# Optimization experiments

Hardware: AMD Instinct MI355X
Metric: run time of the kernel (lower is better)

The kernel has to match this reference:

```python
import jax, jax.numpy as jnp
import numpy as np

B, N, T, D, H = 32, 64, 16, 256, 256  # batch, actors, frames, feat dim, hidden_dim


def setup_inputs() -> dict:
    key = jax.random.key(0)
    ks = jax.random.split(key, 6)
    s = lambda fan: 1.0 / np.sqrt(fan)
    return {
        "x": jax.random.normal(ks[0], (B, N, T, D), jnp.float32),
        "W1_t": jax.random.normal(ks[1], (T * D, H), jnp.float32) * s(T * D),
        "b1_t": jnp.zeros((H,), jnp.float32),
        "W2_t": jax.random.normal(ks[2], (H, H), jnp.float32) * s(H),
        "b2_t": jnp.zeros((H,), jnp.float32),
        "W1_i": jax.random.normal(ks[3], (2 * H, H), jnp.float32) * s(2 * H),
        "b1_i": jnp.zeros((H,), jnp.float32),
        "W2_i": jax.random.normal(ks[4], (H, H), jnp.float32) * s(H),
        "b2_i": jnp.zeros((H,), jnp.float32),
    }


def reference(x, W1_t, b1_t, W2_t, b2_t, W1_i, b1_i, W2_i, b2_i):
    b, n, t, d = x.shape
    # STTR_trans output is immediately detached in the original; modeled as
    # identity + stop_gradient (view(N,B,T,-1) then view-back is a no-op on data).
    pf = jax.lax.stop_gradient(x)  # [B, N, T, D]

    # time_track_projection: MLP(T*D -> H -> H), ReLU between layers, no BN, eval dropout.
    h = jax.nn.relu(pf.reshape(b * n, t * d) @ W1_t + b1_t)
    person_feature = (h @ W2_t + b2_t).reshape(b, n, -1)  # [B, N, H]

    # relation_indexes: row-major enumeration of ordered pairs (i, j), j != i.
    # tem1 row N*i+j holds feature i, tem2 row N*i+j holds feature j.
    ii, jj = np.nonzero(~np.eye(n, dtype=bool))  # each [N*(N-1)], row-major order
    pair = jnp.concatenate(
        [person_feature[:, ii, :], person_feature[:, jj, :]], axis=-1
    )  # [B, N*(N-1), 2H] -- gather avoids materializing the full N*N grid

    # interaction_track_projection: MLP(2H -> H -> H)
    hi = jax.nn.relu(pair @ W1_i + b1_i)
    relation_feature = hi @ W2_i + b2_i  # [B, N*(N-1), H]

    return relation_feature, pf, person_feature
```

## Files before the change

kernel.cpp:

```cpp
#include <hip/hip_runtime.h>
#include <stdint.h>

typedef unsigned short u16;
typedef __attribute__((ext_vector_type(4))) float f32x4;
typedef __attribute__((ext_vector_type(8))) short bf16x8;
typedef __attribute__((ext_vector_type(4))) unsigned short u16x4;

#define DEV static __device__ __forceinline__

DEV u16 f2bf(float f) {
  union { float f; uint32_t u; } v; v.f = f;
  uint32_t u = v.u;
  return (u16)((u + 0x7FFFu + ((u >> 16) & 1u)) >> 16);
}

DEV float bf2f(u16 u) {
  union { uint32_t u; float f; } v; v.u = ((uint32_t)u) << 16;
  return v.f;
}

__global__ __launch_bounds__(256) void k_prep(const float* __restrict__ W1t,
                                              const float* __restrict__ W2t,
                                              const float* __restrict__ W1i,
                                              const float* __restrict__ W2i,
                                              const float* __restrict__ b2t,
                                              const float* __restrict__ b1i,
                                              u16* __restrict__ W1T,
                                              u16* __restrict__ W2iT,
                                              u16* __restrict__ WcatT,
                                              float* __restrict__ biascat) {
  __shared__ u16 tile[64][65];
  __shared__ float col[256];
  int b = blockIdx.x;
  int t = threadIdx.x;
  if (b < 272) {
    const float* in;
    u16* out;
    int R, C, bb;
    if (b < 256) { in = W1t; out = W1T; R = 4096; C = 256; bb = b; }
    else         { in = W2i; out = W2iT; R = 256;  C = 256; bb = b - 256; }
    int tr = (bb >> 2) * 64, tc = (bb & 3) * 64;
    int lr = t & 63;
    #pragma unroll
    for (int it = 0; it < 16; ++it) {
      int r = it * 4 + (t >> 6);
      tile[r][lr] = f2bf(in[(tr + r) * C + tc + lr]);
    }
    __syncthreads();
    #pragma unroll
    for (int it = 0; it < 16; ++it) {
      int c = it * 4 + (t >> 6);
      out[(tc + c) * R + tr + lr] = tile[lr][c];
    }
    return;
  }
  if (b < 1040) {
    int n = b - 272;
    int k = t;
    if (n < 256) {
      WcatT[n * 256 + k] = f2bf(W2t[k * 256 + n]);
      return;
    }
    int off = (n < 512) ? 0 : 256;
    int c = n & 255;
    col[k] = W1i[(off + k) * 256 + c];
    __syncthreads();
    const float* wrow = W2t + k * 256;
    float acc = 0.f;
    #pragma unroll 4
    for (int m = 0; m < 256; ++m) acc += wrow[m] * col[m];
    WcatT[n * 256 + k] = f2bf(acc);
    return;
  }
  int n = (b - 1040) * 256 + t;
  float v;
  if (n < 256) {
    v = b2t[n];
  } else {
    int off = (n < 512) ? 0 : 256;
    int c = n & 255;
    float acc = (n < 512) ? 0.f : b1i[c];
    for (int k = 0; k < 256; ++k) acc += b2t[k] * W1i[(off + k) * 256 + c];
    v = acc;
  }
  biascat[n] = v;
}

__global__ __launch_bounds__(256) void k_gemm1f(const float* __restrict__ x,
                                                float* __restrict__ pf,
                                                const u16* __restrict__ BT,
                                                u16* __restrict__ part) {
  __shared__ u16 As[32][520];
  int t = threadIdx.x;
  int m0 = blockIdx.x * 32;
  int k0 = blockIdx.y * 512;
  {
    int row = t >> 3;
    int cb = (t & 7) * 4;
    const float* src = x + (m0 + row) * 4096 + k0;
    float* dst = pf + (m0 + row) * 4096 + k0;
    #pragma unroll
    for (int j = 0; j < 16; ++j) {
      f32x4 v = *(const f32x4*)(src + cb + j * 32);
      *(f32x4*)(dst + cb + j * 32) = v;
      u16x4 o;
      #pragma unroll
      for (int e = 0; e < 4; ++e) o[e] = f2bf(v[e]);
      *(u16x4*)(&As[row][cb + j * 32]) = o;
    }
  }
  __syncthreads();
  int w = t >> 6, l = t & 63;
  int n0 = w * 64;
  int koff = (l >> 4) * 8;
  const u16* pb0 = BT + (n0 + (l & 15)) * 4096 + k0 + koff;
  int ar = l & 15;
  f32x4 acc[2][4] = {};
  for (int ks = 0; ks < 16; ++ks) {
    bf16x8 a[2], bfr[4];
    #pragma unroll
    for (int mf = 0; mf < 2; ++mf)
      a[mf] = *(const bf16x8*)(&As[ar + mf * 16][koff + ks * 32]);
    #pragma unroll
    for (int nf = 0; nf < 4; ++nf)
      bfr[nf] = *(const bf16x8*)(pb0 + nf * 16 * 4096 + ks * 32);
    #pragma unroll
    for (int mf = 0; mf < 2; ++mf)
      #pragma unroll
      for (int nf = 0; nf < 4; ++nf)
        acc[mf][nf] = __builtin_amdgcn_mfma_f32_16x16x32_bf16(bfr[nf], a[mf], acc[mf][nf], 0, 0, 0);
  }
  u16* out = part + blockIdx.y * (2048 * 256);
  #pragma unroll
  for (int mf = 0; mf < 2; ++mf) {
    int row = m0 + mf * 16 + (l & 15);
    #pragma unroll
    for (int nf = 0; nf < 4; ++nf) {
      int colv = n0 + nf * 16 + ((l >> 4) * 4);
      u16x4 o;
      #pragma unroll
      for (int r = 0; r < 4; ++r) o[r] = f2bf(acc[mf][nf][r]);
      *(u16x4*)(out + row * 256 + colv) = o;
    }
  }
}

__global__ __launch_bounds__(256) void k_reduce_h(const u16* __restrict__ part,
                                                  const float* __restrict__ b1t,
                                                  u16* __restrict__ hb) {
  int i = blockIdx.x * 256 + threadIdx.x;
  int e = i * 4;
  f32x4 s = {};
  #pragma unroll
  for (int z = 0; z < 8; ++z) {
    u16x4 p = *(const u16x4*)(part + z * (2048 * 256) + e);
    #pragma unroll
    for (int r = 0; r < 4; ++r) s[r] += bf2f(p[r]);
  }
  f32x4 bb = *(const f32x4*)(b1t + (e & 255));
  u16x4 o;
  #pragma unroll
  for (int r = 0; r < 4; ++r) o[r] = f2bf(fmaxf(s[r] + bb[r], 0.f));
  *(u16x4*)(hb + e) = o;
}

__global__ __launch_bounds__(256) void k_gemm3(const u16* __restrict__ A,
                                               const u16* __restrict__ BT,
                                               const float* __restrict__ biascat,
                                               float* __restrict__ person,
                                               float* __restrict__ Apr,
                                               float* __restrict__ Bpr) {
  int w = threadIdx.x >> 6, l = threadIdx.x & 63;
  int row = blockIdx.x * 64 + w * 16 + (l & 15);
  int coln = blockIdx.y * 64;
  int k0 = (l >> 4) * 8;
  const u16* pa = A + row * 256 + k0;
  const u16* pb0 = BT + (coln + (l & 15)) * 256 + k0;
  f32x4 acc[4] = {};
  #pragma unroll
  for (int ks = 0; ks < 8; ++ks) {
    bf16x8 a = *(const bf16x8*)(pa + ks * 32);
    #pragma unroll
    for (int nf = 0; nf < 4; ++nf) {
      bf16x8 b = *(const bf16x8*)(pb0 + nf * 16 * 256 + ks * 32);
      acc[nf] = __builtin_amdgcn_mfma_f32_16x16x32_bf16(b, a, acc[nf], 0, 0, 0);
    }
  }
  float* dst;
  int cbase = coln;
  if (coln < 256) { dst = person; }
  else if (coln < 512) { dst = Apr; cbase = coln - 256; }
  else { dst = Bpr; cbase = coln - 512; }
  #pragma unroll
  for (int nf = 0; nf < 4; ++nf) {
    int lc = nf * 16 + ((l >> 4) * 4);
    f32x4 bias4 = *(const f32x4*)(biascat + coln + lc);
    *(f32x4*)(dst + row * 256 + cbase + lc) = acc[nf] + bias4;
  }
}

__global__ __launch_bounds__(512, 2) void k_pair_gemm(const float* __restrict__ Apr,
                                                      const float* __restrict__ Bpr,
                                                      const u16* __restrict__ W2iT,
                                                      const float* __restrict__ b2i,
                                                      float* __restrict__ rel) {
  __shared__ u16 hi[128 * 264];
  int t = threadIdx.x;
  int lane = t & 63;
  int R0 = blockIdx.x * 128;
  #pragma unroll
  for (int it = 0; it < 16; ++it) {
    int r = it * 8 + (t >> 6);
    int R = R0 + r;
    int b = R / 4032;
    int q = R - b * 4032;
    int i = q / 63;
    int rem = q - i * 63;
    int j = rem + (rem >= i ? 1 : 0);
    f32x4 va = *(const f32x4*)(Apr + (b * 64 + i) * 256 + lane * 4);
    f32x4 vb = *(const f32x4*)(Bpr + (b * 64 + j) * 256 + lane * 4);
    u16x4 o;
    #pragma unroll
    for (int e = 0; e < 4; ++e) o[e] = f2bf(fmaxf(va[e] + vb[e], 0.f));
    *(u16x4*)(&hi[r * 264 + lane * 4]) = o;
  }
  __syncthreads();
  int wid = t >> 6;
  int wr = wid >> 2, wc = wid & 3;
  f32x4 acc[4][4] = {};
  int arow0 = wr * 64 + (lane & 15);
  int koff = (lane >> 4) * 8;
  const u16* pb0 = W2iT + (wc * 64 + (lane & 15)) * 256 + koff;
  #pragma unroll 2
  for (int ks = 0; ks < 8; ++ks) {
    bf16x8 a[4], bfr[4];
    #pragma unroll
    for (int mf = 0; mf < 4; ++mf)
      a[mf] = *(const bf16x8*)(&hi[(arow0 + mf * 16) * 264 + ks * 32 + koff]);
    #pragma unroll
    for (int nf = 0; nf < 4; ++nf)
      bfr[nf] = *(const bf16x8*)(pb0 + nf * 16 * 256 + ks * 32);
    #pragma unroll
    for (int mf = 0; mf < 4; ++mf)
      #pragma unroll
      for (int nf = 0; nf < 4; ++nf)
        acc[mf][nf] = __builtin_amdgcn_mfma_f32_16x16x32_bf16(bfr[nf], a[mf], acc[mf][nf], 0, 0, 0);
  }
  f32x4 bias4[4];
  #pragma unroll
  for (int nf = 0; nf < 4; ++nf)
    bias4[nf] = *(const f32x4*)(b2i + wc * 64 + nf * 16 + ((lane >> 4) * 4));
  #pragma unroll
  for (int mf = 0; mf < 4; ++mf) {
    int row = R0 + wr * 64 + mf * 16 + (lane & 15);
    #pragma unroll
    for (int nf = 0; nf < 4; ++nf) {
      int gc = wc * 64 + nf * 16 + ((lane >> 4) * 4);
      *(f32x4*)(rel + row * 256 + gc) = acc[mf][nf] + bias4[nf];
    }
  }
}


extern "C" void kernel_launch(void* const* d_in, const int* in_sizes, int n_in,
                              void* d_out, int out_size, void* d_ws, size_t ws_size,
                              hipStream_t stream) {
  const float* x   = (const float*)d_in[0];
  const float* W1t = (const float*)d_in[1];
  const float* b1t = (const float*)d_in[2];
  const float* W2t = (const float*)d_in[3];
  const float* b2t = (const float*)d_in[4];
  const float* W1i = (const float*)d_in[5];
  const float* b1i = (const float*)d_in[6];
  const float* W2i = (const float*)d_in[7];
  const float* b2i = (const float*)d_in[8];

  float* out = (float*)d_out;
  float* rel = out;
  float* pf = out + 33030144;
  float* person = out + 41418752;

  char* ws = (char*)d_ws;
  u16*   W1T     = (u16*)(ws + 0);
  u16*   WcatT   = (u16*)(ws + 2097152);
  u16*   W2iT    = (u16*)(ws + 2490368);
  float* biascat = (float*)(ws + 2621440);
  u16*   h_bf    = (u16*)(ws + 2625536);
  float* Apr     = (float*)(ws + 3674112);
  float* Bpr     = (float*)(ws + 5771264);
  u16*   part    = (u16*)(ws + 7868416);

  k_prep<<<1043, 256, 0, stream>>>(W1t, W2t, W1i, W2i, b2t, b1i,
                                   W1T, W2iT, WcatT, biascat);
  k_gemm1f<<<dim3(64, 8), 256, 0, stream>>>(x, pf, W1T, part);
  k_reduce_h<<<512, 256, 0, stream>>>(part, b1t, h_bf);
  k_gemm3<<<dim3(32, 12), 256, 0, stream>>>(h_bf, WcatT, biascat, person, Apr, Bpr);
  k_pair_gemm<<<1008, 512, 0, stream>>>(Apr, Bpr, W2iT, b2i, rel);
}
```

Measured before the change: 119.6 us.

## Halve gemm1 row tile, vectorize prep dot product, repad pair-gemm LDS

The first-layer GEMM now uses 16-row tiles instead of 32, doubling the grid to 1024 blocks. This spreads the 33 MB x read/copy across more CUs, but each block now reloads the full W1 slice for half as many rows. The weight-fold dot product in k_prep is vectorized with float4 loads. The LDS row pitch is changed in k_gemm1f (520 to 532) and k_pair_gemm (264 to 276) to alter bank-conflict patterns.

```diff
diff --git a/kernel.cpp b/kernel.cpp
--- a/kernel.cpp
+++ b/kernel.cpp
@@ -66,9 +66,15 @@
     col[k] = W1i[(off + k) * 256 + c];
     __syncthreads();
     const float* wrow = W2t + k * 256;
-    float acc = 0.f;
+    const float* cp = col;
+    f32x4 acc4 = {};
     #pragma unroll 4
-    for (int m = 0; m < 256; ++m) acc += wrow[m] * col[m];
+    for (int m = 0; m < 64; ++m) {
+      f32x4 wv = *(const f32x4*)(wrow + m * 4);
+      f32x4 cv = *(const f32x4*)(cp + m * 4);
+      acc4 += wv * cv;
+    }
+    float acc = acc4[0] + acc4[1] + acc4[2] + acc4[3];
     WcatT[n * 256 + k] = f2bf(acc);
     return;
   }
@@ -90,23 +96,23 @@
                                                 float* __restrict__ pf,
                                                 const u16* __restrict__ BT,
                                                 u16* __restrict__ part) {
-  __shared__ u16 As[32][520];
+  __shared__ u16 As[16][532];
   int t = threadIdx.x;
-  int m0 = blockIdx.x * 32;
+  int m0 = blockIdx.x * 16;
   int k0 = blockIdx.y * 512;
   {
-    int row = t >> 3;
-    int cb = (t & 7) * 4;
+    int row = t >> 4;
+    int cb = (t & 15) * 4;
     const float* src = x + (m0 + row) * 4096 + k0;
     float* dst = pf + (m0 + row) * 4096 + k0;
     #pragma unroll
-    for (int j = 0; j < 16; ++j) {
-      f32x4 v = *(const f32x4*)(src + cb + j * 32);
-      *(f32x4*)(dst + cb + j * 32) = v;
+    for (int j = 0; j < 8; ++j) {
+      f32x4 v = *(const f32x4*)(src + cb + j * 64);
+      *(f32x4*)(dst + cb + j * 64) = v;
       u16x4 o;
       #pragma unroll
       for (int e = 0; e < 4; ++e) o[e] = f2bf(v[e]);
-      *(u16x4*)(&As[row][cb + j * 32]) = o;
+      *(u16x4*)(&As[row][cb + j * 64]) = o;
     }
   }
   __syncthreads();
@@ -115,33 +121,25 @@
   int koff = (l >> 4) * 8;
   const u16* pb0 = BT + (n0 + (l & 15)) * 4096 + k0 + koff;
   int ar = l & 15;
-  f32x4 acc[2][4] = {};
+  f32x4 acc[4] = {};
+  #pragma unroll 4
   for (int ks = 0; ks < 16; ++ks) {
-    bf16x8 a[2], bfr[4];
-    #pragma unroll
-    for (int mf = 0; mf < 2; ++mf)
-      a[mf] = *(const bf16x8*)(&As[ar + mf * 16][koff + ks * 32]);
-    #pragma unroll
-    for (int nf = 0; nf < 4; ++nf)
-      bfr[nf] = *(const bf16x8*)(pb0 + nf * 16 * 4096 + ks * 32);
-    #pragma unroll
-    for (int mf = 0; mf < 2; ++mf)
-      #pragma unroll
-      for (int nf = 0; nf < 4; ++nf)
-        acc[mf][nf] = __builtin_amdgcn_mfma_f32_16x16x32_bf16(bfr[nf], a[mf], acc[mf][nf], 0, 0, 0);
+    bf16x8 a = *(const bf16x8*)(&As[ar][koff + ks * 32]);
+    #pragma unroll
+    for (int nf = 0; nf < 4; ++nf) {
+      bf16x8 b = *(const bf16x8*)(pb0 + nf * 16 * 4096 + ks * 32);
+      acc[nf] = __builtin_amdgcn_mfma_f32_16x16x32_bf16(b, a, acc[nf], 0, 0, 0);
+    }
   }
   u16* out = part + blockIdx.y * (2048 * 256);
-  #pragma unroll
-  for (int mf = 0; mf < 2; ++mf) {
-    int row = m0 + mf * 16 + (l & 15);
-    #pragma unroll
-    for (int nf = 0; nf < 4; ++nf) {
-      int colv = n0 + nf * 16 + ((l >> 4) * 4);
-      u16x4 o;
-      #pragma unroll
-      for (int r = 0; r < 4; ++r) o[r] = f2bf(acc[mf][nf][r]);
-      *(u16x4*)(out + row * 256 + colv) = o;
-    }
+  int orow = m0 + (l & 15);
+  #pragma unroll
+  for (int nf = 0; nf < 4; ++nf) {
+    int colv = n0 + nf * 16 + ((l >> 4) * 4);
+    u16x4 o;
+    #pragma unroll
+    for (int r = 0; r < 4; ++r) o[r] = f2bf(acc[nf][r]);
+    *(u16x4*)(out + orow * 256 + colv) = o;
   }
 }
 
@@ -204,7 +202,7 @@
                                                       const u16* __restrict__ W2iT,
                                                       const float* __restrict__ b2i,
                                                       float* __restrict__ rel) {
-  __shared__ u16 hi[128 * 264];
+  __shared__ u16 hi[128 * 276];
   int t = threadIdx.x;
   int lane = t & 63;
   int R0 = blockIdx.x * 128;
@@ -222,7 +220,7 @@
     u16x4 o;
     #pragma unroll
     for (int e = 0; e < 4; ++e) o[e] = f2bf(fmaxf(va[e] + vb[e], 0.f));
-    *(u16x4*)(&hi[r * 264 + lane * 4]) = o;
+    *(u16x4*)(&hi[r * 276 + lane * 4]) = o;
   }
   __syncthreads();
   int wid = t >> 6;
@@ -236,7 +234,7 @@
     bf16x8 a[4], bfr[4];
     #pragma unroll
     for (int mf = 0; mf < 4; ++mf)
-      a[mf] = *(const bf16x8*)(&hi[(arow0 + mf * 16) * 264 + ks * 32 + koff]);
+      a[mf] = *(const bf16x8*)(&hi[(arow0 + mf * 16) * 276 + ks * 32 + koff]);
     #pragma unroll
     for (int nf = 0; nf < 4; ++nf)
       bfr[nf] = *(const bf16x8*)(pb0 + nf * 16 * 256 + ks * 32);
@@ -292,7 +290,7 @@
 
   k_prep<<<1043, 256, 0, stream>>>(W1t, W2t, W1i, W2i, b2t, b1i,
                                    W1T, W2iT, WcatT, biascat);
-  k_gemm1f<<<dim3(64, 8), 256, 0, stream>>>(x, pf, W1T, part);
+  k_gemm1f<<<dim3(128, 8), 256, 0, stream>>>(x, pf, W1T, part);
   k_reduce_h<<<512, 256, 0, stream>>>(part, b1t, h_bf);
   k_gemm3<<<dim3(32, 12), 256, 0, stream>>>(h_bf, WcatT, biascat, person, Apr, Bpr);
   k_pair_gemm<<<1008, 512, 0, stream>>>(Apr, Bpr, W2iT, b2i, rel);
```

Result: slower. 136.0 us (+13.7%).
